# Kernel tuning notes

Measured on AMD Instinct MI355X. Metric: run time of the kernel, lower is better.

Reference implementation:

```python
import jax, jax.numpy as jnp
import numpy as np

BSZ, D = 256, 512
LOGIT_SCALE = 1.0


def setup_inputs() -> dict:
    key = jax.random.key(0)
    k1, k2, k3 = jax.random.split(key, 3)
    x = jax.random.normal(k1, (BSZ, D), dtype=jnp.float32)
    y = jax.random.normal(k2, (BSZ, D), dtype=jnp.float32)
    z = jax.random.normal(k3, (BSZ, D), dtype=jnp.float32)
    return {"x": x, "y": y, "z": z}


def _logits_n_squared(anchor, a, b, shift):
    # torch recursion: products[i*bsz + r] = a[r] * roll(b, i)[r] = a[r] * b[(r - i) % bsz]
    bsz = anchor.shape[0]
    P = a[None, :, :] * b[shift]              # (i, r, d) = (bsz, bsz, d)
    logits = jnp.einsum('ad,ird->air', anchor, P)  # (a, i, r)
    return LOGIT_SCALE * logits.reshape(bsz, bsz * bsz)


def _cross_entropy_diag(logits):
    bsz = logits.shape[0]
    lp = jax.nn.log_softmax(logits, axis=-1)
    idx = jnp.arange(bsz)
    return -jnp.mean(lp[idx, idx])


def reference(x, y, z):
    bsz = x.shape[0]
    r = jnp.arange(bsz)
    shift = (r[None, :] - r[:, None]) % bsz   # (i, r): index into b after roll by i
    reps = [x, y, z]
    losses = []
    for i in range(3):
        anchor = reps[i]
        non_anchor = [reps[j] for j in range(3) if j != i]
        logits = _logits_n_squared(anchor, non_anchor[0], non_anchor[1], shift)
        losses.append(_cross_entropy_diag(logits))
    return sum(losses) / 3.0
```

## Files before the change

kernel.cpp:

```cpp
#include <hip/hip_runtime.h>

#define DIM 512
#define BK 32
#define ASTRIDE 40

typedef unsigned int uint;
typedef unsigned short ushort;
typedef __attribute__((ext_vector_type(8))) short short8;
typedef __attribute__((ext_vector_type(4))) float f32x4;

#define GLOAD_LDS(g, l) __builtin_amdgcn_global_load_lds( \
    (const __attribute__((address_space(1))) void*)(g), \
    (__attribute__((address_space(3))) void*)(l), 16, 0, 0)

__device__ __forceinline__ uint pack_bf16(float a, float b) {
    union { float f; uint u; } ua, ub;
    ua.f = a; ub.f = b;
    uint x0 = ua.u + 0x8000u;
    uint x1 = ub.u + 0x8000u;
    return __builtin_amdgcn_perm(x1, x0, 0x07060302);
}

__global__ void zconv_kernel(const float* __restrict__ z, ushort* __restrict__ zb) {
    int t = blockIdx.x * 256 + threadIdx.x;
    int f = t * 8;
    float4 a = *(const float4*)(z + f);
    float4 b = *(const float4*)(z + f + 4);
    uint4 o;
    o.x = pack_bf16(a.x, a.y);
    o.y = pack_bf16(a.z, a.w);
    o.z = pack_bf16(b.x, b.y);
    o.w = pack_bf16(b.z, b.w);
    *(uint4*)(zb + f) = o;
}

__global__ void __launch_bounds__(512, 4)
gemm_fused(const float* __restrict__ x, const float* __restrict__ y,
           const ushort* __restrict__ zb, const float* __restrict__ z,
           float* __restrict__ rowM, float* __restrict__ rowS,
           float* __restrict__ colM, float* __restrict__ colS,
           float* __restrict__ diag, uint* __restrict__ counter) {
    __shared__ __align__(16) float xs[DIM];
    __shared__ __align__(16) ushort As[2][128 * ASTRIDE];
    __shared__ __align__(16) ushort Bs[2][256 * BK];
    __shared__ float redA[128 * 4];
    __shared__ float rowMaxS[128];
    __shared__ float redB[256 * 2];
    __shared__ float colMaxS[256];
    __shared__ float dred[8];

    const int tid = threadIdx.x;
    const int a   = blockIdx.x >> 1;
    const int rt  = blockIdx.x & 1;

    if (blockIdx.x == 0 && tid == 0) *counter = 0u;

    xs[tid] = x[a * DIM + tid];

    const int lane = tid & 63;
    const int wave = tid >> 6;
    const int quad = lane >> 4;
    const int ln15 = lane & 15;
    const int wr = wave >> 2;
    const int wc = wave & 3;

    if (rt == 0) {
        float p = xs[tid] * y[a * DIM + tid] * z[a * DIM + tid];
        #pragma unroll
        for (int m = 1; m < 64; m <<= 1) p += __shfl_xor(p, m, 64);
        if (lane == 0) dred[wave] = p;
        __syncthreads();
        if (tid == 0) {
            float s = 0.f;
            #pragma unroll
            for (int w2 = 0; w2 < 8; ++w2) s += dred[w2];
            diag[a] = s;
        }
    }
    __syncthreads();

    f32x4 acc[4][4];
    #pragma unroll
    for (int i = 0; i < 4; ++i)
        #pragma unroll
        for (int j = 0; j < 4; ++j)
            acc[i][j] = (f32x4){0.f, 0.f, 0.f, 0.f};

    const int rA = tid >> 2;
    const int kA = (tid & 3) * 8;
    const float* yrow = y + (rt * 128 + rA) * DIM + kA;

    const int s0 = wave * 128 + lane;
    const int row0 = s0 >> 2, kc0 = ((s0 & 3) - (row0 >> 1)) & 3;
    const ushort* gB0 = zb + row0 * DIM + kc0 * 8;
    const int s1 = s0 + 64;
    const int row1 = s1 >> 2, kc1 = ((s1 & 3) - (row1 >> 1)) & 3;
    const ushort* gB1 = zb + row1 * DIM + kc1 * 8;

    GLOAD_LDS(gB0, &Bs[0][wave * 1024]);
    GLOAD_LDS(gB1, &Bs[0][wave * 1024 + 512]);
    float4 ya = *(const float4*)(yrow);
    float4 yb = *(const float4*)(yrow + 4);
    {
        float4 x0 = *(const float4*)(xs + kA);
        float4 x1 = *(const float4*)(xs + kA + 4);
        uint4 o;
        o.x = pack_bf16(ya.x * x0.x, ya.y * x0.y);
        o.y = pack_bf16(ya.z * x0.z, ya.w * x0.w);
        o.z = pack_bf16(yb.x * x1.x, yb.y * x1.y);
        o.w = pack_bf16(yb.z * x1.z, yb.w * x1.w);
        *(uint4*)(&As[0][rA * ASTRIDE + kA]) = o;
    }
    ya = *(const float4*)(yrow + 32);
    yb = *(const float4*)(yrow + 36);

    #pragma unroll 2
    for (int kt = 0; kt < 16; ++kt) {
        const int cur = kt & 1, nxt = cur ^ 1;
        __syncthreads();
        if (kt < 15) {
            GLOAD_LDS(gB0 + (kt + 1) * 32, &Bs[nxt][wave * 1024]);
            GLOAD_LDS(gB1 + (kt + 1) * 32, &Bs[nxt][wave * 1024 + 512]);
        }
        short8 af[4], bfr[4];
        #pragma unroll
        for (int i = 0; i < 4; ++i)
            af[i] = *(const short8*)(&As[cur][(wr * 64 + i * 16 + ln15) * ASTRIDE + quad * 8]);
        #pragma unroll
        for (int j = 0; j < 4; ++j) {
            int row = wc * 64 + j * 16 + ln15;
            int pos = row * 4 + ((quad + (row >> 1)) & 3);
            bfr[j] = *(const short8*)(&Bs[cur][pos * 8]);
        }
        #pragma unroll
        for (int i = 0; i < 4; ++i)
            #pragma unroll
            for (int j = 0; j < 4; ++j)
                acc[i][j] = __builtin_amdgcn_mfma_f32_16x16x32_bf16(af[i], bfr[j], acc[i][j], 0, 0, 0);
        if (kt < 15) {
            const int k1 = (kt + 1) * 32;
            float4 x0 = *(const float4*)(xs + k1 + kA);
            float4 x1 = *(const float4*)(xs + k1 + kA + 4);
            uint4 o;
            o.x = pack_bf16(ya.x * x0.x, ya.y * x0.y);
            o.y = pack_bf16(ya.z * x0.z, ya.w * x0.w);
            o.z = pack_bf16(yb.x * x1.x, yb.y * x1.y);
            o.w = pack_bf16(yb.z * x1.z, yb.w * x1.w);
            *(uint4*)(&As[nxt][rA * ASTRIDE + kA]) = o;
            if (kt < 14) {
                ya = *(const float4*)(yrow + (kt + 2) * 32);
                yb = *(const float4*)(yrow + (kt + 2) * 32 + 4);
            }
        }
    }
    __syncthreads();

    #pragma unroll
    for (int i = 0; i < 4; ++i) {
        #pragma unroll
        for (int reg = 0; reg < 4; ++reg) {
            float m = fmaxf(fmaxf(acc[i][0][reg], acc[i][1][reg]),
                            fmaxf(acc[i][2][reg], acc[i][3][reg]));
            #pragma unroll
            for (int d = 1; d < 16; d <<= 1) m = fmaxf(m, __shfl_xor(m, d, 64));
            if (ln15 == 0) redA[(wr * 64 + i * 16 + quad * 4 + reg) * 4 + wc] = m;
        }
    }
    __syncthreads();
    if (tid < 128) {
        float m = fmaxf(fmaxf(redA[tid * 4 + 0], redA[tid * 4 + 1]),
                        fmaxf(redA[tid * 4 + 2], redA[tid * 4 + 3]));
        rowMaxS[tid] = m;
    }
    __syncthreads();
    #pragma unroll
    for (int i = 0; i < 4; ++i) {
        #pragma unroll
        for (int reg = 0; reg < 4; ++reg) {
            int r = wr * 64 + i * 16 + quad * 4 + reg;
            float rm = rowMaxS[r];
            float s = __expf(acc[i][0][reg] - rm) + __expf(acc[i][1][reg] - rm)
                    + __expf(acc[i][2][reg] - rm) + __expf(acc[i][3][reg] - rm);
            #pragma unroll
            for (int d = 1; d < 16; d <<= 1) s += __shfl_xor(s, d, 64);
            if (ln15 == 0) redA[r * 4 + wc] = s;
        }
    }
    __syncthreads();
    if (tid < 128) {
        float s = redA[tid * 4 + 0] + redA[tid * 4 + 1] + redA[tid * 4 + 2] + redA[tid * 4 + 3];
        int rg = rt * 128 + tid;
        rowM[a * 256 + rg] = rowMaxS[tid];
        rowS[a * 256 + rg] = s;
    }

    #pragma unroll
    for (int j = 0; j < 4; ++j) {
        float m = -3.4e38f;
        #pragma unroll
        for (int i = 0; i < 4; ++i)
            #pragma unroll
            for (int reg = 0; reg < 4; ++reg)
                m = fmaxf(m, acc[i][j][reg]);
        m = fmaxf(m, __shfl_xor(m, 16, 64));
        m = fmaxf(m, __shfl_xor(m, 32, 64));
        if (quad == 0) redB[(wc * 64 + j * 16 + ln15) * 2 + wr] = m;
    }
    __syncthreads();
    if (tid < 256) colMaxS[tid] = fmaxf(redB[tid * 2], redB[tid * 2 + 1]);
    __syncthreads();
    #pragma unroll
    for (int j = 0; j < 4; ++j) {
        int n = wc * 64 + j * 16 + ln15;
        float cm = colMaxS[n];
        float s = 0.f;
        #pragma unroll
        for (int i = 0; i < 4; ++i)
            #pragma unroll
            for (int reg = 0; reg < 4; ++reg)
                s += __expf(acc[i][j][reg] - cm);
        s += __shfl_xor(s, 16, 64);
        s += __shfl_xor(s, 32, 64);
        if (quad == 0) redB[n * 2 + wr] = s;
    }
    __syncthreads();
    if (tid < 256) {
        float s = redB[tid * 2] + redB[tid * 2 + 1];
        colM[(a * 256 + tid) * 2 + rt] = colMaxS[tid];
        colS[(a * 256 + tid) * 2 + rt] = s;
    }
}

__device__ __forceinline__ float blk_max(float v, float* sm) {
    #pragma unroll
    for (int d = 1; d < 64; d <<= 1) v = fmaxf(v, __shfl_xor(v, d, 64));
    __syncthreads();
    if ((threadIdx.x & 63) == 0) sm[threadIdx.x >> 6] = v;
    __syncthreads();
    return fmaxf(fmaxf(sm[0], sm[1]), fmaxf(sm[2], sm[3]));
}
__device__ __forceinline__ float blk_sum(float v, float* sm) {
    #pragma unroll
    for (int d = 1; d < 64; d <<= 1) v += __shfl_xor(v, d, 64);
    __syncthreads();
    if ((threadIdx.x & 63) == 0) sm[threadIdx.x >> 6] = v;
    __syncthreads();
    return sm[0] + sm[1] + sm[2] + sm[3];
}

__global__ void combine_final(const float* __restrict__ rowM, const float* __restrict__ rowS,
                              const float* __restrict__ colM, const float* __restrict__ colS,
                              const float* __restrict__ diag,
                              float* __restrict__ m123, uint* __restrict__ counter,
                              float* __restrict__ out) {
    __shared__ float sm[4];
    __shared__ uint isLast;
    int b = blockIdx.x, t = threadIdx.x;
    float m = rowM[b * 256 + t], s = rowS[b * 256 + t];
    float M = blk_max(m, sm);
    float S = blk_sum(s * __expf(m - M), sm);
    float M1 = M + __logf(S);
    m = rowM[t * 256 + b]; s = rowS[t * 256 + b];
    M = blk_max(m, sm);
    S = blk_sum(s * __expf(m - M), sm);
    float M2 = M + __logf(S);
    float am = colM[(t * 256 + b) * 2 + 0], av = colS[(t * 256 + b) * 2 + 0];
    float bm = colM[(t * 256 + b) * 2 + 1], bv = colS[(t * 256 + b) * 2 + 1];
    m = fmaxf(am, bm);
    s = av * __expf(am - m) + bv * __expf(bm - m);
    M = blk_max(m, sm);
    S = blk_sum(s * __expf(m - M), sm);
    float M3 = M + __logf(S);
    if (t == 0) {
        m123[b] = M1 + M2 + M3;
        __threadfence();
        isLast = (atomicAdd(counter, 1u) == 255u) ? 1u : 0u;
    }
    __syncthreads();
    if (isLast) {
        __threadfence();
        const volatile float* vm = (const volatile float*)m123;
        const volatile float* vd = (const volatile float*)diag;
        float S1 = blk_sum(vm[t], sm);
        float S2 = blk_sum(vd[t], sm);
        if (t == 0) out[0] = S1 / 768.0f - S2 / 256.0f;
    }
}

extern "C" void kernel_launch(void* const* d_in, const int* in_sizes, int n_in,
                              void* d_out, int out_size, void* d_ws, size_t ws_size,
                              hipStream_t stream) {
    const float* x = (const float*)d_in[0];
    const float* y = (const float*)d_in[1];
    const float* z = (const float*)d_in[2];
    char* w = (char*)d_ws;
    ushort* zb  = (ushort*)(w);
    float* rowM = (float*)(w + 262144);
    float* rowS = (float*)(w + 524288);
    float* colM = (float*)(w + 786432);
    float* colS = (float*)(w + 1310720);
    float* diag = (float*)(w + 1835008);
    float* m123 = (float*)(w + 1836032);
    uint*  counter = (uint*)(w + 1837056);
    float* out  = (float*)d_out;

    zconv_kernel<<<64, 256, 0, stream>>>(z, zb);
    gemm_fused<<<512, 512, 0, stream>>>(x, y, zb, z, rowM, rowS, colM, colS, diag, counter);
    combine_final<<<256, 256, 0, stream>>>(rowM, rowS, colM, colS, diag, m123, counter, out);
}
```

Before: 98.77 us.

## Fuse three kernels into one cooperative kernel with grid syncs

Merges the bf16 conversion of z, the fused GEMM with row/column softmax statistics, and the final combine into a single cooperative launch. Grid-wide syncs replace the kernel boundaries, removing two launch gaps and their tail effects. The cost is two grid barriers, a fallback to the old three-kernel path if the cooperative launch fails, and the requirement that all 512 blocks of 512 threads be co-resident. Only half of the blocks do work in the final phase.

```diff
diff --git a/kernel.cpp b/kernel.cpp
--- a/kernel.cpp
+++ b/kernel.cpp
@@ -1,4 +1,7 @@
 #include <hip/hip_runtime.h>
+#include <hip/hip_cooperative_groups.h>
+
+namespace cg = cooperative_groups;
 
 #define DIM 512
 #define BK 32
@@ -287,6 +290,271 @@
     }
 }
 
+
+__device__ __forceinline__ float blk_max512(float v, float* sm) {
+    #pragma unroll
+    for (int d = 1; d < 64; d <<= 1) v = fmaxf(v, __shfl_xor(v, d, 64));
+    __syncthreads();
+    if (threadIdx.x < 256 && (threadIdx.x & 63) == 0) sm[threadIdx.x >> 6] = v;
+    __syncthreads();
+    return fmaxf(fmaxf(sm[0], sm[1]), fmaxf(sm[2], sm[3]));
+}
+__device__ __forceinline__ float blk_sum512(float v, float* sm) {
+    #pragma unroll
+    for (int d = 1; d < 64; d <<= 1) v += __shfl_xor(v, d, 64);
+    __syncthreads();
+    if (threadIdx.x < 256 && (threadIdx.x & 63) == 0) sm[threadIdx.x >> 6] = v;
+    __syncthreads();
+    return sm[0] + sm[1] + sm[2] + sm[3];
+}
+
+__global__ void __launch_bounds__(512, 4)
+fused_all(const float* __restrict__ x, const float* __restrict__ y,
+          const float* __restrict__ z, ushort* __restrict__ zb,
+          float* __restrict__ rowM, float* __restrict__ rowS,
+          float* __restrict__ colM, float* __restrict__ colS,
+          float* __restrict__ diag, float* __restrict__ m123,
+          uint* __restrict__ counter, float* __restrict__ out) {
+    __shared__ __align__(16) float xs[DIM];
+    __shared__ __align__(16) ushort As[2][128 * ASTRIDE];
+    __shared__ __align__(16) ushort Bs[2][256 * BK];
+    __shared__ float redA[128 * 4];
+    __shared__ float rowMaxS[128];
+    __shared__ float redB[256 * 2];
+    __shared__ float colMaxS[256];
+    __shared__ float dred[8];
+    __shared__ uint isLastS;
+
+    const int tid = threadIdx.x;
+    const int a   = blockIdx.x >> 1;
+    const int rt  = blockIdx.x & 1;
+
+    if (blockIdx.x < 128) {
+        int idx = blockIdx.x * 512 + tid;
+        float2 v = *(const float2*)(z + idx * 2);
+        ((uint*)zb)[idx] = pack_bf16(v.x, v.y);
+    }
+    if (blockIdx.x == 0 && tid == 0) *counter = 0u;
+
+    xs[tid] = x[a * DIM + tid];
+
+    const int lane = tid & 63;
+    const int wave = tid >> 6;
+    const int quad = lane >> 4;
+    const int ln15 = lane & 15;
+    const int wr = wave >> 2;
+    const int wc = wave & 3;
+
+    if (rt == 0) {
+        float p = xs[tid] * y[a * DIM + tid] * z[a * DIM + tid];
+        #pragma unroll
+        for (int m = 1; m < 64; m <<= 1) p += __shfl_xor(p, m, 64);
+        if (lane == 0) dred[wave] = p;
+        __syncthreads();
+        if (tid == 0) {
+            float s = 0.f;
+            #pragma unroll
+            for (int w2 = 0; w2 < 8; ++w2) s += dred[w2];
+            diag[a] = s;
+        }
+    }
+    __syncthreads();
+
+    cg::this_grid().sync();
+
+    f32x4 acc[4][4];
+    #pragma unroll
+    for (int i = 0; i < 4; ++i)
+        #pragma unroll
+        for (int j = 0; j < 4; ++j)
+            acc[i][j] = (f32x4){0.f, 0.f, 0.f, 0.f};
+
+    const int rA = tid >> 2;
+    const int kA = (tid & 3) * 8;
+    const float* yrow = y + (rt * 128 + rA) * DIM + kA;
+
+    const int s0 = wave * 128 + lane;
+    const int row0 = s0 >> 2, kc0 = ((s0 & 3) - (row0 >> 1)) & 3;
+    const ushort* gB0 = zb + row0 * DIM + kc0 * 8;
+    const int s1 = s0 + 64;
+    const int row1 = s1 >> 2, kc1 = ((s1 & 3) - (row1 >> 1)) & 3;
+    const ushort* gB1 = zb + row1 * DIM + kc1 * 8;
+
+    GLOAD_LDS(gB0, &Bs[0][wave * 1024]);
+    GLOAD_LDS(gB1, &Bs[0][wave * 1024 + 512]);
+    float4 ya = *(const float4*)(yrow);
+    float4 yb = *(const float4*)(yrow + 4);
+    {
+        float4 x0 = *(const float4*)(xs + kA);
+        float4 x1 = *(const float4*)(xs + kA + 4);
+        uint4 o;
+        o.x = pack_bf16(ya.x * x0.x, ya.y * x0.y);
+        o.y = pack_bf16(ya.z * x0.z, ya.w * x0.w);
+        o.z = pack_bf16(yb.x * x1.x, yb.y * x1.y);
+        o.w = pack_bf16(yb.z * x1.z, yb.w * x1.w);
+        *(uint4*)(&As[0][rA * ASTRIDE + kA]) = o;
+    }
+    ya = *(const float4*)(yrow + 32);
+    yb = *(const float4*)(yrow + 36);
+
+    #pragma unroll 2
+    for (int kt = 0; kt < 16; ++kt) {
+        const int cur = kt & 1, nxt = cur ^ 1;
+        __syncthreads();
+        if (kt < 15) {
+            GLOAD_LDS(gB0 + (kt + 1) * 32, &Bs[nxt][wave * 1024]);
+            GLOAD_LDS(gB1 + (kt + 1) * 32, &Bs[nxt][wave * 1024 + 512]);
+        }
+        short8 af[4], bfr[4];
+        #pragma unroll
+        for (int i = 0; i < 4; ++i)
+            af[i] = *(const short8*)(&As[cur][(wr * 64 + i * 16 + ln15) * ASTRIDE + quad * 8]);
+        #pragma unroll
+        for (int j = 0; j < 4; ++j) {
+            int row = wc * 64 + j * 16 + ln15;
+            int pos = row * 4 + ((quad + (row >> 1)) & 3);
+            bfr[j] = *(const short8*)(&Bs[cur][pos * 8]);
+        }
+        #pragma unroll
+        for (int i = 0; i < 4; ++i)
+            #pragma unroll
+            for (int j = 0; j < 4; ++j)
+                acc[i][j] = __builtin_amdgcn_mfma_f32_16x16x32_bf16(af[i], bfr[j], acc[i][j], 0, 0, 0);
+        if (kt < 15) {
+            const int k1 = (kt + 1) * 32;
+            float4 x0 = *(const float4*)(xs + k1 + kA);
+            float4 x1 = *(const float4*)(xs + k1 + kA + 4);
+            uint4 o;
+            o.x = pack_bf16(ya.x * x0.x, ya.y * x0.y);
+            o.y = pack_bf16(ya.z * x0.z, ya.w * x0.w);
+            o.z = pack_bf16(yb.x * x1.x, yb.y * x1.y);
+            o.w = pack_bf16(yb.z * x1.z, yb.w * x1.w);
+            *(uint4*)(&As[nxt][rA * ASTRIDE + kA]) = o;
+            if (kt < 14) {
+                ya = *(const float4*)(yrow + (kt + 2) * 32);
+                yb = *(const float4*)(yrow + (kt + 2) * 32 + 4);
+            }
+        }
+    }
+    __syncthreads();
+
+    #pragma unroll
+    for (int i = 0; i < 4; ++i) {
+        #pragma unroll
+        for (int reg = 0; reg < 4; ++reg) {
+            float m = fmaxf(fmaxf(acc[i][0][reg], acc[i][1][reg]),
+                            fmaxf(acc[i][2][reg], acc[i][3][reg]));
+            #pragma unroll
+            for (int d = 1; d < 16; d <<= 1) m = fmaxf(m, __shfl_xor(m, d, 64));
+            if (ln15 == 0) redA[(wr * 64 + i * 16 + quad * 4 + reg) * 4 + wc] = m;
+        }
+    }
+    __syncthreads();
+    if (tid < 128) {
+        float m = fmaxf(fmaxf(redA[tid * 4 + 0], redA[tid * 4 + 1]),
+                        fmaxf(redA[tid * 4 + 2], redA[tid * 4 + 3]));
+        rowMaxS[tid] = m;
+    }
+    __syncthreads();
+    #pragma unroll
+    for (int i = 0; i < 4; ++i) {
+        #pragma unroll
+        for (int reg = 0; reg < 4; ++reg) {
+            int r = wr * 64 + i * 16 + quad * 4 + reg;
+            float rm = rowMaxS[r];
+            float s = __expf(acc[i][0][reg] - rm) + __expf(acc[i][1][reg] - rm)
+                    + __expf(acc[i][2][reg] - rm) + __expf(acc[i][3][reg] - rm);
+            #pragma unroll
+            for (int d = 1; d < 16; d <<= 1) s += __shfl_xor(s, d, 64);
+            if (ln15 == 0) redA[r * 4 + wc] = s;
+        }
+    }
+    __syncthreads();
+    if (tid < 128) {
+        float s = redA[tid * 4 + 0] + redA[tid * 4 + 1] + redA[tid * 4 + 2] + redA[tid * 4 + 3];
+        int rg = rt * 128 + tid;
+        rowM[a * 256 + rg] = rowMaxS[tid];
+        rowS[a * 256 + rg] = s;
+    }
+
+    #pragma unroll
+    for (int j = 0; j < 4; ++j) {
+        float m = -3.4e38f;
+        #pragma unroll
+        for (int i = 0; i < 4; ++i)
+            #pragma unroll
+            for (int reg = 0; reg < 4; ++reg)
+                m = fmaxf(m, acc[i][j][reg]);
+        m = fmaxf(m, __shfl_xor(m, 16, 64));
+        m = fmaxf(m, __shfl_xor(m, 32, 64));
+        if (quad == 0) redB[(wc * 64 + j * 16 + ln15) * 2 + wr] = m;
+    }
+    __syncthreads();
+    if (tid < 256) colMaxS[tid] = fmaxf(redB[tid * 2], redB[tid * 2 + 1]);
+    __syncthreads();
+    #pragma unroll
+    for (int j = 0; j < 4; ++j) {
+        int n = wc * 64 + j * 16 + ln15;
+        float cm = colMaxS[n];
+        float s = 0.f;
+        #pragma unroll
+        for (int i = 0; i < 4; ++i)
+            #pragma unroll
+            for (int reg = 0; reg < 4; ++reg)
+                s += __expf(acc[i][j][reg] - cm);
+        s += __shfl_xor(s, 16, 64);
+        s += __shfl_xor(s, 32, 64);
+        if (quad == 0) redB[n * 2 + wr] = s;
+    }
+    __syncthreads();
+    if (tid < 256) {
+        float s = redB[tid * 2] + redB[tid * 2 + 1];
+        colM[(a * 256 + tid) * 2 + rt] = colMaxS[tid];
+        colS[(a * 256 + tid) * 2 + rt] = s;
+    }
+
+    cg::this_grid().sync();
+
+    if (rt == 0) {
+        const int b = a;
+        const int t = tid;
+        const bool act = t < 256;
+        float m = act ? rowM[b * 256 + t] : -3.4e38f;
+        float s = act ? rowS[b * 256 + t] : 0.f;
+        float M = blk_max512(m, dred);
+        float S = blk_sum512(act ? s * __expf(m - M) : 0.f, dred);
+        float M1 = M + __logf(S);
+        m = act ? rowM[t * 256 + b] : -3.4e38f;
+        s = act ? rowS[t * 256 + b] : 0.f;
+        M = blk_max512(m, dred);
+        S = blk_sum512(act ? s * __expf(m - M) : 0.f, dred);
+        float M2 = M + __logf(S);
+        float am = act ? colM[(t * 256 + b) * 2 + 0] : -3.4e38f;
+        float av = act ? colS[(t * 256 + b) * 2 + 0] : 0.f;
+        float bm = act ? colM[(t * 256 + b) * 2 + 1] : -3.4e38f;
+        float bv = act ? colS[(t * 256 + b) * 2 + 1] : 0.f;
+        m = fmaxf(am, bm);
+        s = av * __expf(am - m) + bv * __expf(bm - m);
+        M = blk_max512(m, dred);
+        S = blk_sum512(act ? s * __expf(m - M) : 0.f, dred);
+        float M3 = M + __logf(S);
+        if (t == 0) {
+            m123[b] = M1 + M2 + M3;
+            __threadfence();
+            isLastS = (atomicAdd(counter, 1u) == 255u) ? 1u : 0u;
+        }
+        __syncthreads();
+        if (isLastS) {
+            __threadfence();
+            const volatile float* vm = (const volatile float*)m123;
+            const volatile float* vd = (const volatile float*)diag;
+            float S1 = blk_sum512(act ? vm[t] : 0.f, dred);
+            float S2 = blk_sum512(act ? vd[t] : 0.f, dred);
+            if (t == 0) out[0] = S1 / 768.0f - S2 / 256.0f;
+        }
+    }
+}
+
 extern "C" void kernel_launch(void* const* d_in, const int* in_sizes, int n_in,
                               void* d_out, int out_size, void* d_ws, size_t ws_size,
                               hipStream_t stream) {
@@ -304,7 +572,16 @@
     uint*  counter = (uint*)(w + 1837056);
     float* out  = (float*)d_out;
 
-    zconv_kernel<<<64, 256, 0, stream>>>(z, zb);
-    gemm_fused<<<512, 512, 0, stream>>>(x, y, zb, z, rowM, rowS, colM, colS, diag, counter);
-    combine_final<<<256, 256, 0, stream>>>(rowM, rowS, colM, colS, diag, m123, counter, out);
-}
+    void* args[12] = {(void*)&x, (void*)&y, (void*)&z, (void*)&zb,
+                      (void*)&rowM, (void*)&rowS, (void*)&colM, (void*)&colS,
+                      (void*)&diag, (void*)&m123, (void*)&counter, (void*)&out};
+    hipError_t err = hipLaunchCooperativeKernel((const void*)fused_all,
+                                                dim3(512), dim3(512),
+                                                args, 0u, stream);
+    if (err != hipSuccess) {
+        (void)hipGetLastError();
+        zconv_kernel<<<64, 256, 0, stream>>>(z, zb);
+        gemm_fused<<<512, 512, 0, stream>>>(x, y, zb, z, rowM, rowS, colM, colS, diag, counter);
+        combine_final<<<256, 256, 0, stream>>>(rowM, rowS, colM, colS, diag, m123, counter, out);
+    }
+}
```

After: 227.1 us. 2.3x slower.

## Fuse final combine into GEMM kernel via last-arriving blocks spin-waiting

Applied to the files above, without the earlier changes.

Removes the separate combine_final launch. The last 32 gemm_fused blocks to finish, ranked by an atomic counter, spin until all 512 blocks are done. Each then reduces 8 of the 256 rows, and a second counter picks the block that computes the final loss. The counter reset moves into zconv_kernel. This saves a kernel launch and its gap, but relies on all blocks becoming resident (512 blocks at 4 per CU) to avoid deadlock, and it serializes the combine work onto 32 blocks.

```diff
diff --git a/kernel.cpp b/kernel.cpp
--- a/kernel.cpp
+++ b/kernel.cpp
@@ -3,6 +3,8 @@
 #define DIM 512
 #define BK 32
 #define ASTRIDE 40
+#define NCOMB 32
+#define RTHRESH (512 - NCOMB)
 
 typedef unsigned int uint;
 typedef unsigned short ushort;
@@ -21,7 +23,9 @@
     return __builtin_amdgcn_perm(x1, x0, 0x07060302);
 }
 
-__global__ void zconv_kernel(const float* __restrict__ z, ushort* __restrict__ zb) {
+__global__ void zconv_kernel(const float* __restrict__ z, ushort* __restrict__ zb,
+                             uint* __restrict__ cnt) {
+    if (blockIdx.x == 0 && threadIdx.x == 0) { cnt[0] = 0u; cnt[1] = 0u; }
     int t = blockIdx.x * 256 + threadIdx.x;
     int f = t * 8;
     float4 a = *(const float4*)(z + f);
@@ -34,12 +38,30 @@
     *(uint4*)(zb + f) = o;
 }
 
+__device__ __forceinline__ float blk_max512(float v, float* sm) {
+    #pragma unroll
+    for (int d = 1; d < 64; d <<= 1) v = fmaxf(v, __shfl_xor(v, d, 64));
+    __syncthreads();
+    if (threadIdx.x < 256 && (threadIdx.x & 63) == 0) sm[threadIdx.x >> 6] = v;
+    __syncthreads();
+    return fmaxf(fmaxf(sm[0], sm[1]), fmaxf(sm[2], sm[3]));
+}
+__device__ __forceinline__ float blk_sum512(float v, float* sm) {
+    #pragma unroll
+    for (int d = 1; d < 64; d <<= 1) v += __shfl_xor(v, d, 64);
+    __syncthreads();
+    if (threadIdx.x < 256 && (threadIdx.x & 63) == 0) sm[threadIdx.x >> 6] = v;
+    __syncthreads();
+    return sm[0] + sm[1] + sm[2] + sm[3];
+}
+
 __global__ void __launch_bounds__(512, 4)
 gemm_fused(const float* __restrict__ x, const float* __restrict__ y,
            const ushort* __restrict__ zb, const float* __restrict__ z,
            float* __restrict__ rowM, float* __restrict__ rowS,
            float* __restrict__ colM, float* __restrict__ colS,
-           float* __restrict__ diag, uint* __restrict__ counter) {
+           float* __restrict__ diag, float* __restrict__ m123,
+           uint* __restrict__ cnt, float* __restrict__ out) {
     __shared__ __align__(16) float xs[DIM];
     __shared__ __align__(16) ushort As[2][128 * ASTRIDE];
     __shared__ __align__(16) ushort Bs[2][256 * BK];
@@ -48,12 +70,12 @@
     __shared__ float redB[256 * 2];
     __shared__ float colMaxS[256];
     __shared__ float dred[8];
+    __shared__ uint rankS;
+    __shared__ uint lastS;
 
     const int tid = threadIdx.x;
     const int a   = blockIdx.x >> 1;
     const int rt  = blockIdx.x & 1;
-
-    if (blockIdx.x == 0 && tid == 0) *counter = 0u;
 
     xs[tid] = x[a * DIM + tid];
 
@@ -229,61 +251,70 @@
         colM[(a * 256 + tid) * 2 + rt] = colMaxS[tid];
         colS[(a * 256 + tid) * 2 + rt] = s;
     }
-}
-
-__device__ __forceinline__ float blk_max(float v, float* sm) {
-    #pragma unroll
-    for (int d = 1; d < 64; d <<= 1) v = fmaxf(v, __shfl_xor(v, d, 64));
-    __syncthreads();
-    if ((threadIdx.x & 63) == 0) sm[threadIdx.x >> 6] = v;
-    __syncthreads();
-    return fmaxf(fmaxf(sm[0], sm[1]), fmaxf(sm[2], sm[3]));
-}
-__device__ __forceinline__ float blk_sum(float v, float* sm) {
-    #pragma unroll
-    for (int d = 1; d < 64; d <<= 1) v += __shfl_xor(v, d, 64);
-    __syncthreads();
-    if ((threadIdx.x & 63) == 0) sm[threadIdx.x >> 6] = v;
-    __syncthreads();
-    return sm[0] + sm[1] + sm[2] + sm[3];
-}
-
-__global__ void combine_final(const float* __restrict__ rowM, const float* __restrict__ rowS,
-                              const float* __restrict__ colM, const float* __restrict__ colS,
-                              const float* __restrict__ diag,
-                              float* __restrict__ m123, uint* __restrict__ counter,
-                              float* __restrict__ out) {
-    __shared__ float sm[4];
-    __shared__ uint isLast;
-    int b = blockIdx.x, t = threadIdx.x;
-    float m = rowM[b * 256 + t], s = rowS[b * 256 + t];
-    float M = blk_max(m, sm);
-    float S = blk_sum(s * __expf(m - M), sm);
-    float M1 = M + __logf(S);
-    m = rowM[t * 256 + b]; s = rowS[t * 256 + b];
-    M = blk_max(m, sm);
-    S = blk_sum(s * __expf(m - M), sm);
-    float M2 = M + __logf(S);
-    float am = colM[(t * 256 + b) * 2 + 0], av = colS[(t * 256 + b) * 2 + 0];
-    float bm = colM[(t * 256 + b) * 2 + 1], bv = colS[(t * 256 + b) * 2 + 1];
-    m = fmaxf(am, bm);
-    s = av * __expf(am - m) + bv * __expf(bm - m);
-    M = blk_max(m, sm);
-    S = blk_sum(s * __expf(m - M), sm);
-    float M3 = M + __logf(S);
-    if (t == 0) {
-        m123[b] = M1 + M2 + M3;
+
+    __syncthreads();
+    if (tid == 0) {
         __threadfence();
-        isLast = (atomicAdd(counter, 1u) == 255u) ? 1u : 0u;
-    }
-    __syncthreads();
-    if (isLast) {
+        rankS = atomicAdd(&cnt[0], 1u);
+    }
+    __syncthreads();
+    const uint rank = rankS;
+    if (rank < (uint)RTHRESH) return;
+
+    if (tid == 0) {
+        while (__hip_atomic_load(&cnt[0], __ATOMIC_RELAXED, __HIP_MEMORY_SCOPE_AGENT) < 512u) {
+            __builtin_amdgcn_s_sleep(1);
+        }
+    }
+    __syncthreads();
+    __threadfence();
+
+    const volatile float* vRowM = (const volatile float*)rowM;
+    const volatile float* vRowS = (const volatile float*)rowS;
+    const volatile float* vColM = (const volatile float*)colM;
+    const volatile float* vColS = (const volatile float*)colS;
+
+    const int bBase = (int)(rank - (uint)RTHRESH) * (256 / NCOMB);
+    #pragma unroll 1
+    for (int k = 0; k < 256 / NCOMB; ++k) {
+        const int b = bBase + k;
+        const int t = tid;
+        const bool act = t < 256;
+        float m = act ? vRowM[b * 256 + t] : -3.4e38f;
+        float s = act ? vRowS[b * 256 + t] : 0.f;
+        float M = blk_max512(m, dred);
+        float S = blk_sum512(act ? s * __expf(m - M) : 0.f, dred);
+        float M1 = M + __logf(S);
+        m = act ? vRowM[t * 256 + b] : -3.4e38f;
+        s = act ? vRowS[t * 256 + b] : 0.f;
+        M = blk_max512(m, dred);
+        S = blk_sum512(act ? s * __expf(m - M) : 0.f, dred);
+        float M2 = M + __logf(S);
+        float am = act ? vColM[(t * 256 + b) * 2 + 0] : -3.4e38f;
+        float av = act ? vColS[(t * 256 + b) * 2 + 0] : 0.f;
+        float bm = act ? vColM[(t * 256 + b) * 2 + 1] : -3.4e38f;
+        float bv = act ? vColS[(t * 256 + b) * 2 + 1] : 0.f;
+        m = fmaxf(am, bm);
+        s = av * __expf(am - m) + bv * __expf(bm - m);
+        M = blk_max512(m, dred);
+        S = blk_sum512(act ? s * __expf(m - M) : 0.f, dred);
+        float M3 = M + __logf(S);
+        if (t == 0) m123[b] = M1 + M2 + M3;
+        __syncthreads();
+    }
+
+    if (tid == 0) {
+        __threadfence();
+        lastS = (atomicAdd(&cnt[1], 1u) == (uint)(NCOMB - 1)) ? 1u : 0u;
+    }
+    __syncthreads();
+    if (lastS) {
         __threadfence();
         const volatile float* vm = (const volatile float*)m123;
         const volatile float* vd = (const volatile float*)diag;
-        float S1 = blk_sum(vm[t], sm);
-        float S2 = blk_sum(vd[t], sm);
-        if (t == 0) out[0] = S1 / 768.0f - S2 / 256.0f;
+        float S1 = blk_sum512(tid < 256 ? vm[tid] : 0.f, dred);
+        float S2 = blk_sum512(tid < 256 ? vd[tid] : 0.f, dred);
+        if (tid == 0) out[0] = S1 / 768.0f - S2 / 256.0f;
     }
 }
 
@@ -301,10 +332,10 @@
     float* colS = (float*)(w + 1310720);
     float* diag = (float*)(w + 1835008);
     float* m123 = (float*)(w + 1836032);
-    uint*  counter = (uint*)(w + 1837056);
+    uint*  cnt  = (uint*)(w + 1837056);
     float* out  = (float*)d_out;
 
-    zconv_kernel<<<64, 256, 0, stream>>>(z, zb);
-    gemm_fused<<<512, 512, 0, stream>>>(x, y, zb, z, rowM, rowS, colM, colS, diag, counter);
-    combine_final<<<256, 256, 0, stream>>>(rowM, rowS, colM, colS, diag, m123, counter, out);
-}
+    zconv_kernel<<<64, 256, 0, stream>>>(z, zb, cnt);
+    gemm_fused<<<512, 512, 0, stream>>>(x, y, zb, z, rowM, rowS, colM, colS,
+                                        diag, m123, cnt, out);
+}
```

Result: slower. 148.8 us (+50.6%).

## Fuse z bf16 conversion into GEMM B-tile staging and drop zconv kernel

Applied to the files above, without the earlier changes.

Removes the separate zconv kernel launch and instead has each GEMM block load fp32 z rows through registers, pack them to bf16 and write them into the swizzled B shared-memory tile, replacing the direct global-to-LDS loads. Adds s_setprio around the MFMA block and loads A fragments per row-tile rather than all up front, which lowers register use. The aim is to save one kernel launch and the zb round trip through memory. In exchange every one of the 512 blocks now reads and converts fp32 z, which doubles B global traffic and adds VALU pack work per k-step.

```diff
diff --git a/kernel.cpp b/kernel.cpp
--- a/kernel.cpp
+++ b/kernel.cpp
@@ -8,10 +8,6 @@
 typedef unsigned short ushort;
 typedef __attribute__((ext_vector_type(8))) short short8;
 typedef __attribute__((ext_vector_type(4))) float f32x4;
-
-#define GLOAD_LDS(g, l) __builtin_amdgcn_global_load_lds( \
-    (const __attribute__((address_space(1))) void*)(g), \
-    (__attribute__((address_space(3))) void*)(l), 16, 0, 0)
 
 __device__ __forceinline__ uint pack_bf16(float a, float b) {
     union { float f; uint u; } ua, ub;
@@ -21,22 +17,9 @@
     return __builtin_amdgcn_perm(x1, x0, 0x07060302);
 }
 
-__global__ void zconv_kernel(const float* __restrict__ z, ushort* __restrict__ zb) {
-    int t = blockIdx.x * 256 + threadIdx.x;
-    int f = t * 8;
-    float4 a = *(const float4*)(z + f);
-    float4 b = *(const float4*)(z + f + 4);
-    uint4 o;
-    o.x = pack_bf16(a.x, a.y);
-    o.y = pack_bf16(a.z, a.w);
-    o.z = pack_bf16(b.x, b.y);
-    o.w = pack_bf16(b.z, b.w);
-    *(uint4*)(zb + f) = o;
-}
-
 __global__ void __launch_bounds__(512, 4)
 gemm_fused(const float* __restrict__ x, const float* __restrict__ y,
-           const ushort* __restrict__ zb, const float* __restrict__ z,
+           const float* __restrict__ z,
            float* __restrict__ rowM, float* __restrict__ rowS,
            float* __restrict__ colM, float* __restrict__ colS,
            float* __restrict__ diag, uint* __restrict__ counter) {
@@ -64,6 +47,24 @@
     const int wr = wave >> 2;
     const int wc = wave & 3;
 
+    const int rA = tid >> 2;
+    const int kA = (tid & 3) * 8;
+    const float* yrow = y + (rt * 128 + rA) * DIM + kA;
+
+    const int s0 = wave * 128 + lane;
+    const int row0 = s0 >> 2, kc0 = ((s0 & 3) - (row0 >> 1)) & 3;
+    const float* gz0 = z + row0 * DIM + kc0 * 8;
+    const int s1 = s0 + 64;
+    const int row1 = s1 >> 2, kc1 = ((s1 & 3) - (row1 >> 1)) & 3;
+    const float* gz1 = z + row1 * DIM + kc1 * 8;
+
+    float4 ya  = *(const float4*)(yrow);
+    float4 yb  = *(const float4*)(yrow + 4);
+    float4 z0a = *(const float4*)(gz0);
+    float4 z0b = *(const float4*)(gz0 + 4);
+    float4 z1a = *(const float4*)(gz1);
+    float4 z1b = *(const float4*)(gz1 + 4);
+
     if (rt == 0) {
         float p = xs[tid] * y[a * DIM + tid] * z[a * DIM + tid];
         #pragma unroll
@@ -86,21 +87,6 @@
         for (int j = 0; j < 4; ++j)
             acc[i][j] = (f32x4){0.f, 0.f, 0.f, 0.f};
 
-    const int rA = tid >> 2;
-    const int kA = (tid & 3) * 8;
-    const float* yrow = y + (rt * 128 + rA) * DIM + kA;
-
-    const int s0 = wave * 128 + lane;
-    const int row0 = s0 >> 2, kc0 = ((s0 & 3) - (row0 >> 1)) & 3;
-    const ushort* gB0 = zb + row0 * DIM + kc0 * 8;
-    const int s1 = s0 + 64;
-    const int row1 = s1 >> 2, kc1 = ((s1 & 3) - (row1 >> 1)) & 3;
-    const ushort* gB1 = zb + row1 * DIM + kc1 * 8;
-
-    GLOAD_LDS(gB0, &Bs[0][wave * 1024]);
-    GLOAD_LDS(gB1, &Bs[0][wave * 1024 + 512]);
-    float4 ya = *(const float4*)(yrow);
-    float4 yb = *(const float4*)(yrow + 4);
     {
         float4 x0 = *(const float4*)(xs + kA);
         float4 x1 = *(const float4*)(xs + kA + 4);
@@ -110,33 +96,45 @@
         o.z = pack_bf16(yb.x * x1.x, yb.y * x1.y);
         o.w = pack_bf16(yb.z * x1.z, yb.w * x1.w);
         *(uint4*)(&As[0][rA * ASTRIDE + kA]) = o;
-    }
-    ya = *(const float4*)(yrow + 32);
-    yb = *(const float4*)(yrow + 36);
+        uint4 ob;
+        ob.x = pack_bf16(z0a.x, z0a.y);
+        ob.y = pack_bf16(z0a.z, z0a.w);
+        ob.z = pack_bf16(z0b.x, z0b.y);
+        ob.w = pack_bf16(z0b.z, z0b.w);
+        *(uint4*)(&Bs[0][s0 * 8]) = ob;
+        ob.x = pack_bf16(z1a.x, z1a.y);
+        ob.y = pack_bf16(z1a.z, z1a.w);
+        ob.z = pack_bf16(z1b.x, z1b.y);
+        ob.w = pack_bf16(z1b.z, z1b.w);
+        *(uint4*)(&Bs[0][s1 * 8]) = ob;
+    }
+    ya  = *(const float4*)(yrow + 32);
+    yb  = *(const float4*)(yrow + 36);
+    z0a = *(const float4*)(gz0 + 32);
+    z0b = *(const float4*)(gz0 + 36);
+    z1a = *(const float4*)(gz1 + 32);
+    z1b = *(const float4*)(gz1 + 36);
 
     #pragma unroll 2
     for (int kt = 0; kt < 16; ++kt) {
         const int cur = kt & 1, nxt = cur ^ 1;
         __syncthreads();
-        if (kt < 15) {
-            GLOAD_LDS(gB0 + (kt + 1) * 32, &Bs[nxt][wave * 1024]);
-            GLOAD_LDS(gB1 + (kt + 1) * 32, &Bs[nxt][wave * 1024 + 512]);
-        }
-        short8 af[4], bfr[4];
-        #pragma unroll
-        for (int i = 0; i < 4; ++i)
-            af[i] = *(const short8*)(&As[cur][(wr * 64 + i * 16 + ln15) * ASTRIDE + quad * 8]);
+        short8 bfr[4];
         #pragma unroll
         for (int j = 0; j < 4; ++j) {
             int row = wc * 64 + j * 16 + ln15;
             int pos = row * 4 + ((quad + (row >> 1)) & 3);
             bfr[j] = *(const short8*)(&Bs[cur][pos * 8]);
         }
-        #pragma unroll
-        for (int i = 0; i < 4; ++i)
+        __builtin_amdgcn_s_setprio(1);
+        #pragma unroll
+        for (int i = 0; i < 4; ++i) {
+            short8 af = *(const short8*)(&As[cur][(wr * 64 + i * 16 + ln15) * ASTRIDE + quad * 8]);
             #pragma unroll
             for (int j = 0; j < 4; ++j)
-                acc[i][j] = __builtin_amdgcn_mfma_f32_16x16x32_bf16(af[i], bfr[j], acc[i][j], 0, 0, 0);
+                acc[i][j] = __builtin_amdgcn_mfma_f32_16x16x32_bf16(af, bfr[j], acc[i][j], 0, 0, 0);
+        }
+        __builtin_amdgcn_s_setprio(0);
         if (kt < 15) {
             const int k1 = (kt + 1) * 32;
             float4 x0 = *(const float4*)(xs + k1 + kA);
@@ -147,9 +145,24 @@
             o.z = pack_bf16(yb.x * x1.x, yb.y * x1.y);
             o.w = pack_bf16(yb.z * x1.z, yb.w * x1.w);
             *(uint4*)(&As[nxt][rA * ASTRIDE + kA]) = o;
+            uint4 ob;
+            ob.x = pack_bf16(z0a.x, z0a.y);
+            ob.y = pack_bf16(z0a.z, z0a.w);
+            ob.z = pack_bf16(z0b.x, z0b.y);
+            ob.w = pack_bf16(z0b.z, z0b.w);
+            *(uint4*)(&Bs[nxt][s0 * 8]) = ob;
+            ob.x = pack_bf16(z1a.x, z1a.y);
+            ob.y = pack_bf16(z1a.z, z1a.w);
+            ob.z = pack_bf16(z1b.x, z1b.y);
+            ob.w = pack_bf16(z1b.z, z1b.w);
+            *(uint4*)(&Bs[nxt][s1 * 8]) = ob;
             if (kt < 14) {
-                ya = *(const float4*)(yrow + (kt + 2) * 32);
-                yb = *(const float4*)(yrow + (kt + 2) * 32 + 4);
+                ya  = *(const float4*)(yrow + (kt + 2) * 32);
+                yb  = *(const float4*)(yrow + (kt + 2) * 32 + 4);
+                z0a = *(const float4*)(gz0 + (kt + 2) * 32);
+                z0b = *(const float4*)(gz0 + (kt + 2) * 32 + 4);
+                z1a = *(const float4*)(gz1 + (kt + 2) * 32);
+                z1b = *(const float4*)(gz1 + (kt + 2) * 32 + 4);
             }
         }
     }
@@ -294,7 +307,6 @@
     const float* y = (const float*)d_in[1];
     const float* z = (const float*)d_in[2];
     char* w = (char*)d_ws;
-    ushort* zb  = (ushort*)(w);
     float* rowM = (float*)(w + 262144);
     float* rowS = (float*)(w + 524288);
     float* colM = (float*)(w + 786432);
@@ -304,7 +316,6 @@
     uint*  counter = (uint*)(w + 1837056);
     float* out  = (float*)d_out;
 
-    zconv_kernel<<<64, 256, 0, stream>>>(z, zb);
-    gemm_fused<<<512, 512, 0, stream>>>(x, y, zb, z, rowM, rowS, colM, colS, diag, counter);
+    gemm_fused<<<512, 512, 0, stream>>>(x, y, z, rowM, rowS, colM, colS, diag, counter);
     combine_final<<<256, 256, 0, stream>>>(rowM, rowS, colM, colS, diag, m123, counter, out);
 }
```

New measurement: 98.84 us. Within noise of the previous version (+0.1%).
